# Optimization experiments

Measured on AMD Instinct MI355X. Metric: run time of the kernel, lower is better.

The kernel has to match this reference:

```python
import jax, jax.numpy as jnp
import numpy as np

E = 16          # n_routed_experts
Z = 8           # zero_expert_num
K = 4           # moe_topk
H = 1024        # hidden_size
I = 768         # moe_intermediate_size
T = 2048        # tokens
SCALE = 2.5     # routed_scaling_factor


def setup_inputs() -> dict:
    key = jax.random.key(0)
    ks = jax.random.split(key, 6)
    return {
        "hidden_states": jax.random.normal(ks[0], (T, H), dtype=jnp.float32),
        "num_global_tokens": T,
        "max_num_tokens_per_gpu": T,
        "w_router": jax.random.normal(ks[1], (E + Z, H), dtype=jnp.float32) * 0.02,
        "correction_bias": jnp.zeros((E + Z,), dtype=jnp.float32),
        "wg": jax.random.normal(ks[2], (E, I, H), dtype=jnp.float32) * 0.02,
        "wu": jax.random.normal(ks[3], (E, I, H), dtype=jnp.float32) * 0.02,
        "wd": jax.random.normal(ks[4], (E, H, I), dtype=jnp.float32) * 0.02,
    }


def reference(hidden_states, num_global_tokens, max_num_tokens_per_gpu,
              w_router, correction_bias, wg, wu, wd):
    x = hidden_states
    # ---- router gemm (always fp32) ----
    logits = x.astype(jnp.float32) @ w_router.T                      # [T, E+Z]
    # ---- DeepSeekV3-style top-k: sigmoid scores, bias only for selection ----
    scores = jax.nn.sigmoid(logits)
    _, topk_ids = jax.lax.top_k(scores + correction_bias[None, :], K)  # [T, K]
    w = jnp.take_along_axis(scores, topk_ids, axis=-1)               # [T, K]
    w = w / jnp.sum(w, axis=-1, keepdims=True)                       # renormalize
    w = w * SCALE                                                    # routed_scaling_factor
    # ---- zero-expert masking (identity type) ----
    zero_mask = topk_ids >= E                                        # [T, K]
    zero_w = jnp.sum(jnp.where(zero_mask, w, 0.0), axis=-1, keepdims=True)
    ids = jnp.where(zero_mask, 0, topk_ids)
    w = jnp.where(zero_mask, 0.0, w)
    # ---- combine weights per (token, expert); masked slots add 0.0 ----
    cw = jnp.zeros((x.shape[0], E), dtype=jnp.float32)
    cw = cw.at[jnp.arange(x.shape[0])[:, None], ids].add(w)          # [T, E]
    # ---- grouped silu-gated expert MLPs (dense compute + masked combine) ----
    g = jnp.einsum('th,eih->eti', x, wg)                             # [E, T, I]
    u = jnp.einsum('th,eih->eti', x, wu)
    a = jax.nn.silu(g) * u
    y = jnp.einsum('eti,ehi->eth', a, wd)                            # [E, T, H]
    routed = jnp.einsum('eth,te->th', y, cw)                         # [T, H]
    return routed + x * zero_w.astype(x.dtype)
```

## Files before the change

### kernel.cpp

```cpp
#include <hip/hip_runtime.h>
#include <hip/hip_bf16.h>
#include <math.h>

typedef __bf16 bf16x8 __attribute__((ext_vector_type(8)));
typedef float f32x4 __attribute__((ext_vector_type(4)));

#define T_TOK 2048
#define HD 1024
#define ID 768
#define NE 16
#define NEZ 24
#define NK 4
#define SCALE_F 2.5f

#define MFMA(a, b, c) __builtin_amdgcn_mfma_f32_16x16x32_bf16(a, b, c, 0, 0, 0)

__device__ __forceinline__ unsigned short f2bf(float f) {
  unsigned int u = __builtin_bit_cast(unsigned int, f);
  u += 0x7FFFu + ((u >> 16) & 1u);
  return (unsigned short)(u >> 16);
}

__device__ __forceinline__ bf16x8 cvt8(float4 a, float4 b) {
  bf16x8 t;
  t[0] = (__bf16)a.x; t[1] = (__bf16)a.y; t[2] = (__bf16)a.z; t[3] = (__bf16)a.w;
  t[4] = (__bf16)b.x; t[5] = (__bf16)b.y; t[6] = (__bf16)b.z; t[7] = (__bf16)b.w;
  return t;
}

__device__ __forceinline__ void gload16(const void* g, void* l) {
  __builtin_amdgcn_global_load_lds(
      (const __attribute__((address_space(1))) void*)(unsigned long long)(uintptr_t)g,
      (__attribute__((address_space(3))) void*)(uintptr_t)l, 16, 0, 0);
}

__global__ __launch_bounds__(256) void router_k(
    const float* __restrict__ x, const float* __restrict__ wr,
    const float* __restrict__ bias,
    int* __restrict__ counts, int* __restrict__ lists, float* __restrict__ wlist,
    unsigned short* __restrict__ xb, float* __restrict__ out) {
  const int wave = threadIdx.x >> 6, l = threadIdx.x & 63;
  const int t = blockIdx.x * 4 + wave;

  float4 xr[4];
#pragma unroll
  for (int c = 0; c < 4; ++c)
    xr[c] = *(const float4*)(x + (size_t)t * HD + c * 256 + l * 4);
#pragma unroll
  for (int c = 0; c < 4; ++c) {
    ushort4 h;
    h.x = f2bf(xr[c].x); h.y = f2bf(xr[c].y); h.z = f2bf(xr[c].z); h.w = f2bf(xr[c].w);
    *(ushort4*)(xb + (size_t)t * HD + c * 256 + l * 4) = h;
  }

  float acc[NEZ];
#pragma unroll 4
  for (int e = 0; e < NEZ; ++e) {
    float4 s = {0.f, 0.f, 0.f, 0.f};
#pragma unroll
    for (int c = 0; c < 4; ++c) {
      float4 w4 = *(const float4*)(wr + (size_t)e * HD + c * 256 + l * 4);
      s.x = fmaf(w4.x, xr[c].x, s.x); s.y = fmaf(w4.y, xr[c].y, s.y);
      s.z = fmaf(w4.z, xr[c].z, s.z); s.w = fmaf(w4.w, xr[c].w, s.w);
    }
    acc[e] = (s.x + s.y) + (s.z + s.w);
  }
#pragma unroll
  for (int s = 1; s < 64; s <<= 1) {
#pragma unroll
    for (int e = 0; e < NEZ; ++e) acc[e] += __shfl_xor(acc[e], s);
  }
  float sc[NEZ], scb[NEZ];
#pragma unroll
  for (int e = 0; e < NEZ; ++e) {
    float s = 1.f / (1.f + expf(-acc[e]));
    sc[e] = s;
    scb[e] = s + bias[e];
  }
  unsigned picked = 0;
  int ids[NK]; float wv[NK]; float ssum = 0.f;
#pragma unroll
  for (int k = 0; k < NK; ++k) {
    int best = 0; float bv = -1e30f; float bsc = 0.f;
#pragma unroll
    for (int e = 0; e < NEZ; ++e) {
      bool take = (((picked >> e) & 1u) == 0) && (scb[e] > bv);
      best = take ? e : best;
      bv = take ? scb[e] : bv;
      bsc = take ? sc[e] : bsc;
    }
    picked |= 1u << best;
    ids[k] = best; wv[k] = bsc; ssum += bsc;
  }
  const float inv = SCALE_F / ssum;
  float zw = 0.f;
#pragma unroll
  for (int k = 0; k < NK; ++k)
    zw += (ids[k] >= NE) ? wv[k] * inv : 0.f;
  if (l < NK) {
    int id = ids[l];
    if (id < NE) {
      int p = atomicAdd(&counts[id], 1);
      lists[id * T_TOK + p] = t;
      wlist[id * T_TOK + p] = wv[l] * inv;
    }
  }
#pragma unroll
  for (int c = 0; c < 4; ++c) {
    float4 o;
    o.x = xr[c].x * zw; o.y = xr[c].y * zw;
    o.z = xr[c].z * zw; o.w = xr[c].w * zw;
    *(float4*)(out + (size_t)t * HD + c * 256 + l * 4) = o;
  }
}

__global__ __launch_bounds__(256, 3) void gu_k(
    const unsigned short* __restrict__ xb,
    const float* __restrict__ wg, const float* __restrict__ wu,
    const int* __restrict__ counts,
    const int* __restrict__ lists, unsigned short* __restrict__ abuf) {
  const int b = blockIdx.x;
  const int L = (b & 7) * 384 + (b >> 3);
  const int e = L / 192;
  const int rem = L % 192;
  const int xs = rem / 16, ys = rem % 16;
  const int cnt = counts[e];
  const int m0 = ys * 128;
  if (m0 >= cnt) return;
  const int n0 = xs * 64;

  int offs_e = 0;
  for (int i = 0; i < e; ++i) offs_e += counts[i];

  __shared__ int toks[128];
  __shared__ char lds[2][24576];

  const int tid = threadIdx.x;
  if (tid < 128) {
    int m = m0 + tid;
    toks[tid] = (m < cnt) ? lists[e * T_TOK + m] : 0;
  }
  __syncthreads();

  const unsigned short* asrc[2];
#pragma unroll
  for (int j = 0; j < 2; ++j) {
    int row = j * 64 + (tid >> 2);
    int c = ((tid & 3) - (row >> 1)) & 3;
    asrc[j] = xb + (size_t)toks[row] * HD + c * 8;
  }
  const size_t wbase = (size_t)e * ID * HD;
  const float* gsrc[2]; const float* usrc[2];
#pragma unroll
  for (int j = 0; j < 2; ++j) {
    int row = j * 32 + (tid >> 3);
    int c = ((tid & 7) - row) & 7;
    size_t ro = wbase + (size_t)(n0 + row) * HD + c * 4;
    gsrc[j] = wg + ro; usrc[j] = wu + ro;
  }

  const int wid = tid >> 6, l = tid & 63;
  const int wm = (wid >> 1) * 64, wn = (wid & 1) * 32;
  const int q = l >> 4, r = l & 15;

  f32x4 ag[4][2] = {}; f32x4 au[4][2] = {};

  auto stage = [&](int bb, int k0) {
    char* dst = &lds[bb][0] + tid * 16;
#pragma unroll
    for (int j = 0; j < 2; ++j) {
      gload16(asrc[j] + k0, dst + j * 4096);
      gload16(gsrc[j] + k0, dst + 8192 + j * 4096);
      gload16(usrc[j] + k0, dst + 16384 + j * 4096);
    }
  };
  auto comp = [&](int bb) {
    const char* base = &lds[bb][0];
    bf16x8 a[4];
#pragma unroll
    for (int fm = 0; fm < 4; ++fm) {
      int rr = wm + fm * 16 + r;
      int p = (q + (rr >> 1)) & 3;
      a[fm] = *(const bf16x8*)(base + rr * 64 + p * 16);
    }
#pragma unroll
    for (int fn = 0; fn < 2; ++fn) {
      int cc = wn + fn * 16 + r;
      int p0 = (2 * q + cc) & 7, p1 = (2 * q + 1 + cc) & 7;
      const char* pg = base + 8192 + cc * 128;
      const char* pu = base + 16384 + cc * 128;
      float4 g0 = *(const float4*)(pg + p0 * 16);
      float4 g1 = *(const float4*)(pg + p1 * 16);
      float4 u0 = *(const float4*)(pu + p0 * 16);
      float4 u1 = *(const float4*)(pu + p1 * 16);
      bf16x8 bg = cvt8(g0, g1), bu = cvt8(u0, u1);
#pragma unroll
      for (int fm = 0; fm < 4; ++fm) {
        ag[fm][fn] = MFMA(a[fm], bg, ag[fm][fn]);
        au[fm][fn] = MFMA(a[fm], bu, au[fm][fn]);
      }
    }
  };

  stage(0, 0);
  __syncthreads();
  for (int t = 0; t < 32; t += 2) {
    stage(1, (t + 1) * 32);
    comp(0);
    __syncthreads();
    if (t + 2 < 32) stage(0, (t + 2) * 32);
    comp(1);
    __syncthreads();
  }

  const int rowbase = offs_e + m0;
#pragma unroll
  for (int fm = 0; fm < 4; ++fm)
#pragma unroll
    for (int fn = 0; fn < 2; ++fn)
#pragma unroll
      for (int i2 = 0; i2 < 4; ++i2) {
        int mr = wm + fm * 16 + q * 4 + i2;
        if (m0 + mr < cnt) {
          float g = ag[fm][fn][i2], u = au[fm][fn][i2];
          float s = 1.0f / (1.0f + expf(-g));
          float aa = g * s * u;
          int col = n0 + wn + fn * 16 + r;
          abuf[(size_t)(rowbase + mr) * ID + col] = f2bf(aa);
        }
      }
}

__global__ __launch_bounds__(256, 4) void dn_k(
    const unsigned short* __restrict__ abuf,
    const float* __restrict__ wd,
    const int* __restrict__ counts,
    const int* __restrict__ lists, const float* __restrict__ wlist,
    float* __restrict__ out) {
  const int b = blockIdx.x;
  const int L = (b & 7) * 512 + (b >> 3);
  const int e = L / 256;
  const int rem = L % 256;
  const int xs = rem / 16, ys = rem % 16;
  const int cnt = counts[e];
  const int m0 = ys * 128;
  if (m0 >= cnt) return;
  const int n0 = xs * 64;

  int offs_e = 0;
  for (int i = 0; i < e; ++i) offs_e += counts[i];

  __shared__ char lds[2][16384];

  const int tid = threadIdx.x;

  const unsigned short* asrc[2];
#pragma unroll
  for (int j = 0; j < 2; ++j) {
    int row = j * 64 + (tid >> 2);
    int c = ((tid & 3) - (row >> 1)) & 3;
    int m = m0 + row; if (m >= cnt) m = cnt - 1;
    asrc[j] = abuf + (size_t)(offs_e + m) * ID + c * 8;
  }
  const float* bsrc[2];
#pragma unroll
  for (int j = 0; j < 2; ++j) {
    int u = j * 256 + tid;
    int row = u >> 3;
    int c = ((u & 7) - row) & 7;
    bsrc[j] = wd + (size_t)e * HD * ID + (size_t)(n0 + row) * ID + c * 4;
  }

  const int wid = tid >> 6, l = tid & 63;
  const int wm = (wid >> 1) * 64, wn = (wid & 1) * 32;
  const int q = l >> 4, r = l & 15;

  f32x4 acc[4][2] = {};

  auto stage = [&](int bb, int k0) {
    char* dst = &lds[bb][0] + tid * 16;
#pragma unroll
    for (int j = 0; j < 2; ++j) {
      gload16(asrc[j] + k0, dst + j * 4096);
      gload16(bsrc[j] + k0, dst + 8192 + j * 4096);
    }
  };
  auto comp = [&](int bb) {
    const char* base = &lds[bb][0];
    bf16x8 a[4];
#pragma unroll
    for (int fm = 0; fm < 4; ++fm) {
      int rr = wm + fm * 16 + r;
      int p = (q + (rr >> 1)) & 3;
      a[fm] = *(const bf16x8*)(base + rr * 64 + p * 16);
    }
#pragma unroll
    for (int fn = 0; fn < 2; ++fn) {
      int cc = wn + fn * 16 + r;
      int p0 = (2 * q + cc) & 7, p1 = (2 * q + 1 + cc) & 7;
      const char* pb = base + 8192 + cc * 128;
      float4 b0 = *(const float4*)(pb + p0 * 16);
      float4 b1 = *(const float4*)(pb + p1 * 16);
      bf16x8 bb2 = cvt8(b0, b1);
#pragma unroll
      for (int fm = 0; fm < 4; ++fm)
        acc[fm][fn] = MFMA(a[fm], bb2, acc[fm][fn]);
    }
  };

  stage(0, 0);
  __syncthreads();
  for (int t = 0; t < 24; t += 2) {
    stage(1, (t + 1) * 32);
    comp(0);
    __syncthreads();
    if (t + 2 < 24) stage(0, (t + 2) * 32);
    comp(1);
    __syncthreads();
  }

#pragma unroll
  for (int fm = 0; fm < 4; ++fm) {
#pragma unroll
    for (int i2 = 0; i2 < 4; ++i2) {
      int mr = wm + fm * 16 + q * 4 + i2;
      if (m0 + mr < cnt) {
        int tok = lists[e * T_TOK + m0 + mr];
        float wt = wlist[e * T_TOK + m0 + mr];
#pragma unroll
        for (int fn = 0; fn < 2; ++fn) {
          int col = n0 + wn + fn * 16 + r;
          atomicAdd(&out[(size_t)tok * HD + col], acc[fm][fn][i2] * wt);
        }
      }
    }
  }
}

extern "C" void kernel_launch(void* const* d_in, const int* in_sizes, int n_in,
                              void* d_out, int out_size, void* d_ws, size_t ws_size,
                              hipStream_t stream) {
  (void)in_sizes; (void)n_in; (void)out_size; (void)ws_size;
  const float* x    = (const float*)d_in[0];
  const float* wr   = (const float*)d_in[3];
  const float* bias = (const float*)d_in[4];
  const float* wg   = (const float*)d_in[5];
  const float* wu   = (const float*)d_in[6];
  const float* wd   = (const float*)d_in[7];
  float* out = (float*)d_out;

  char* p = (char*)d_ws;
  auto alloc = [&](size_t bytes) {
    char* r = p;
    p += (bytes + 255) & ~(size_t)255;
    return r;
  };
  int*   counts  = (int*)alloc(NE * 4);
  int*   lists   = (int*)alloc((size_t)NE * T_TOK * 4);
  float* wlist   = (float*)alloc((size_t)NE * T_TOK * 4);
  unsigned short* xb   = (unsigned short*)alloc((size_t)T_TOK * HD * 2);
  unsigned short* abuf = (unsigned short*)alloc((size_t)(T_TOK * NK + 128) * ID * 2);

  hipMemsetAsync(counts, 0, NE * 4, stream);
  router_k<<<T_TOK / 4, 256, 0, stream>>>(x, wr, bias, counts, lists, wlist, xb, out);
  gu_k<<<3072, 256, 0, stream>>>(xb, wg, wu, counts, lists, abuf);
  dn_k<<<4096, 256, 0, stream>>>(abuf, wd, counts, lists, wlist, out);
}
```

Before: 128.1 us.

## Keep two LDS stages in flight using partial vmcnt waits and raw barriers

Both grouped GEMM kernels now issue two global-to-LDS stages up front and, each iteration, wait only until the older stage's loads are done (vmcnt 6 or 4) before computing on it, then refill that buffer two steps ahead. The full __syncthreads drains are replaced by explicit s_waitcnt and s_barrier, so the next stage's loads overlap the current compute. The hand-chosen vmcnt values must match the exact number of global_load_lds instructions each stage issues; if the compiler emits other vector memory ops in between, the waits may be too weak and produce races.

```diff
diff --git a/kernel.cpp b/kernel.cpp
--- a/kernel.cpp
+++ b/kernel.cpp
@@ -14,6 +14,10 @@
 #define SCALE_F 2.5f
 
 #define MFMA(a, b, c) __builtin_amdgcn_mfma_f32_16x16x32_bf16(a, b, c, 0, 0, 0)
+#define ASM_VMCNT6() asm volatile("s_waitcnt vmcnt(6)" ::: "memory")
+#define ASM_VMCNT4() asm volatile("s_waitcnt vmcnt(4)" ::: "memory")
+#define ASM_VMCNT0() asm volatile("s_waitcnt vmcnt(0)" ::: "memory")
+#define ASM_BAR()    asm volatile("s_barrier" ::: "memory")
 
 __device__ __forceinline__ unsigned short f2bf(float f) {
   unsigned int u = __builtin_bit_cast(unsigned int, f);
@@ -203,14 +207,13 @@
   };
 
   stage(0, 0);
-  __syncthreads();
-  for (int t = 0; t < 32; t += 2) {
-    stage(1, (t + 1) * 32);
-    comp(0);
-    __syncthreads();
-    if (t + 2 < 32) stage(0, (t + 2) * 32);
-    comp(1);
-    __syncthreads();
+  stage(1, 32);
+  for (int t = 0; t < 32; ++t) {
+    if (t < 31) { ASM_VMCNT6(); } else { ASM_VMCNT0(); }
+    ASM_BAR();
+    comp(t & 1);
+    ASM_BAR();
+    if (t <= 29) stage(t & 1, (t + 2) * 32);
   }
 
   const int rowbase = offs_e + m0;
@@ -309,14 +312,13 @@
   };
 
   stage(0, 0);
-  __syncthreads();
-  for (int t = 0; t < 24; t += 2) {
-    stage(1, (t + 1) * 32);
-    comp(0);
-    __syncthreads();
-    if (t + 2 < 24) stage(0, (t + 2) * 32);
-    comp(1);
-    __syncthreads();
+  stage(1, 32);
+  for (int t = 0; t < 24; ++t) {
+    if (t < 23) { ASM_VMCNT4(); } else { ASM_VMCNT0(); }
+    ASM_BAR();
+    comp(t & 1);
+    ASM_BAR();
+    if (t <= 21) stage(t & 1, (t + 2) * 32);
   }
 
 #pragma unroll
```

New measurement: 128.2 us. About the same (+0.0%).

## Pre-convert down-proj weights to bf16 inside gate/up kernel, widen dn K-tile

Applied to the files above, without the earlier changes.

Appends 512 extra blocks to the gate/up kernel that convert the fp32 down-projection weights to a bf16 workspace buffer, filling otherwise idle tail slots. The down kernel then loads bf16 weights directly, dropping the per-tile fp32-to-bf16 conversion and halving weight traffic. Its K step doubles to 64, with a new swizzled LDS layout and 48KB of LDS, and occupancy is lowered to 3. The cost is an extra full write and reread of the converted weights each call, plus lower occupancy in the down kernel.

```diff
diff --git a/kernel.cpp b/kernel.cpp
--- a/kernel.cpp
+++ b/kernel.cpp
@@ -117,9 +117,21 @@
 __global__ __launch_bounds__(256, 3) void gu_k(
     const unsigned short* __restrict__ xb,
     const float* __restrict__ wg, const float* __restrict__ wu,
+    const float* __restrict__ wd, unsigned short* __restrict__ wdb,
     const int* __restrict__ counts,
     const int* __restrict__ lists, unsigned short* __restrict__ abuf) {
   const int b = blockIdx.x;
+  if (b >= 3072) {
+    const size_t base = (size_t)(b - 3072) * 24576 + threadIdx.x * 4;
+#pragma unroll
+    for (int i = 0; i < 24; ++i) {
+      float4 v = *(const float4*)(wd + base + (size_t)i * 1024);
+      ushort4 h;
+      h.x = f2bf(v.x); h.y = f2bf(v.y); h.z = f2bf(v.z); h.w = f2bf(v.w);
+      *(ushort4*)(wdb + base + (size_t)i * 1024) = h;
+    }
+    return;
+  }
   const int L = (b & 7) * 384 + (b >> 3);
   const int e = L / 192;
   const int rem = L % 192;
@@ -231,9 +243,9 @@
       }
 }
 
-__global__ __launch_bounds__(256, 4) void dn_k(
+__global__ __launch_bounds__(256, 3) void dn_k(
     const unsigned short* __restrict__ abuf,
-    const float* __restrict__ wd,
+    const unsigned short* __restrict__ wdb,
     const int* __restrict__ counts,
     const int* __restrict__ lists, const float* __restrict__ wlist,
     float* __restrict__ out) {
@@ -250,25 +262,26 @@
   int offs_e = 0;
   for (int i = 0; i < e; ++i) offs_e += counts[i];
 
-  __shared__ char lds[2][16384];
+  __shared__ char lds[2][24576];
 
   const int tid = threadIdx.x;
 
-  const unsigned short* asrc[2];
-#pragma unroll
-  for (int j = 0; j < 2; ++j) {
-    int row = j * 64 + (tid >> 2);
-    int c = ((tid & 3) - (row >> 1)) & 3;
+  const unsigned short* asrc[4];
+#pragma unroll
+  for (int j = 0; j < 4; ++j) {
+    int u = j * 256 + tid;
+    int row = u >> 3;
+    int c = ((u & 7) - row) & 7;
     int m = m0 + row; if (m >= cnt) m = cnt - 1;
     asrc[j] = abuf + (size_t)(offs_e + m) * ID + c * 8;
   }
-  const float* bsrc[2];
+  const unsigned short* bsrc[2];
 #pragma unroll
   for (int j = 0; j < 2; ++j) {
     int u = j * 256 + tid;
     int row = u >> 3;
     int c = ((u & 7) - row) & 7;
-    bsrc[j] = wd + (size_t)e * HD * ID + (size_t)(n0 + row) * ID + c * 4;
+    bsrc[j] = wdb + (size_t)e * HD * ID + (size_t)(n0 + row) * ID + c * 8;
   }
 
   const int wid = tid >> 6, l = tid & 63;
@@ -280,41 +293,40 @@
   auto stage = [&](int bb, int k0) {
     char* dst = &lds[bb][0] + tid * 16;
 #pragma unroll
-    for (int j = 0; j < 2; ++j) {
-      gload16(asrc[j] + k0, dst + j * 4096);
-      gload16(bsrc[j] + k0, dst + 8192 + j * 4096);
-    }
+    for (int j = 0; j < 4; ++j) gload16(asrc[j] + k0, dst + j * 4096);
+#pragma unroll
+    for (int j = 0; j < 2; ++j) gload16(bsrc[j] + k0, dst + 16384 + j * 4096);
   };
   auto comp = [&](int bb) {
     const char* base = &lds[bb][0];
-    bf16x8 a[4];
-#pragma unroll
-    for (int fm = 0; fm < 4; ++fm) {
-      int rr = wm + fm * 16 + r;
-      int p = (q + (rr >> 1)) & 3;
-      a[fm] = *(const bf16x8*)(base + rr * 64 + p * 16);
-    }
-#pragma unroll
-    for (int fn = 0; fn < 2; ++fn) {
-      int cc = wn + fn * 16 + r;
-      int p0 = (2 * q + cc) & 7, p1 = (2 * q + 1 + cc) & 7;
-      const char* pb = base + 8192 + cc * 128;
-      float4 b0 = *(const float4*)(pb + p0 * 16);
-      float4 b1 = *(const float4*)(pb + p1 * 16);
-      bf16x8 bb2 = cvt8(b0, b1);
-#pragma unroll
-      for (int fm = 0; fm < 4; ++fm)
-        acc[fm][fn] = MFMA(a[fm], bb2, acc[fm][fn]);
+#pragma unroll
+    for (int kk = 0; kk < 2; ++kk) {
+      bf16x8 a[4];
+#pragma unroll
+      for (int fm = 0; fm < 4; ++fm) {
+        int rr = wm + fm * 16 + r;
+        int kc = kk * 4 + q;
+        a[fm] = *(const bf16x8*)(base + rr * 128 + (((kc + rr) & 7) << 4));
+      }
+#pragma unroll
+      for (int fn = 0; fn < 2; ++fn) {
+        int cc = wn + fn * 16 + r;
+        int kc = kk * 4 + q;
+        bf16x8 bb2 = *(const bf16x8*)(base + 16384 + cc * 128 + (((kc + cc) & 7) << 4));
+#pragma unroll
+        for (int fm = 0; fm < 4; ++fm)
+          acc[fm][fn] = MFMA(a[fm], bb2, acc[fm][fn]);
+      }
     }
   };
 
   stage(0, 0);
   __syncthreads();
-  for (int t = 0; t < 24; t += 2) {
-    stage(1, (t + 1) * 32);
+  for (int t = 0; t < 12; t += 2) {
+    stage(1, (t + 1) * 64);
     comp(0);
     __syncthreads();
-    if (t + 2 < 24) stage(0, (t + 2) * 32);
+    if (t + 2 < 12) stage(0, (t + 2) * 64);
     comp(1);
     __syncthreads();
   }
@@ -360,9 +372,10 @@
   float* wlist   = (float*)alloc((size_t)NE * T_TOK * 4);
   unsigned short* xb   = (unsigned short*)alloc((size_t)T_TOK * HD * 2);
   unsigned short* abuf = (unsigned short*)alloc((size_t)(T_TOK * NK + 128) * ID * 2);
+  unsigned short* wdb  = (unsigned short*)alloc((size_t)NE * HD * ID * 2);
 
   hipMemsetAsync(counts, 0, NE * 4, stream);
   router_k<<<T_TOK / 4, 256, 0, stream>>>(x, wr, bias, counts, lists, wlist, xb, out);
-  gu_k<<<3072, 256, 0, stream>>>(xb, wg, wu, counts, lists, abuf);
-  dn_k<<<4096, 256, 0, stream>>>(abuf, wd, counts, lists, wlist, out);
-}
+  gu_k<<<3584, 256, 0, stream>>>(xb, wg, wu, wd, wdb, counts, lists, abuf);
+  dn_k<<<4096, 256, 0, stream>>>(abuf, wdb, counts, lists, wlist, out);
+}
```

Result: slower. 131.8 us (+2.9%).
